# Performance work log

Measured on AMD Instinct MI355X. Metric: run time of the kernel, lower is better.

## Reference

```python
import jax, jax.numpy as jnp
import numpy as np

EPS = 1e-7
TWO_PI = 2.0 * np.pi

K = 4096   # num gaussians
R = 8192   # num rays
MAP_SIZE = 100


def setup_inputs() -> dict:
    key = jax.random.key(0)
    k1, k2, k3, k4, k5, k6 = jax.random.split(key, 6)
    pos_raw = jax.random.normal(k1, (K, 2), dtype=jnp.float32)            # pre-sigmoid positions
    conc_raw = jax.random.normal(k2, (K,), dtype=jnp.float32)             # pre-softplus concentration
    scale_raw = 0.1 * jax.random.normal(k3, (K, 2), dtype=jnp.float32)    # log-scales
    rot_raw = jax.random.uniform(k4, (K,), dtype=jnp.float32) * TWO_PI    # rotation angles
    p_rays = jax.random.uniform(k5, (R, 2), dtype=jnp.float32) * MAP_SIZE # ray origins in map coords
    u = jax.random.normal(k6, (R, 2), dtype=jnp.float32)
    u_rays = u / jnp.linalg.norm(u, axis=-1, keepdims=True)               # unit ray directions
    return {"pos_raw": pos_raw, "conc_raw": conc_raw, "scale_raw": scale_raw,
            "rot_raw": rot_raw, "p_rays": p_rays, "u_rays": u_rays,
            "map_size": MAP_SIZE}


def _forward(pos_raw, conc_raw, scale_raw, rot_raw, p_rays, u_rays, map_size):
    # --- per-gaussian activations (GasSplattingModel getters) ---
    pos = jax.nn.sigmoid(pos_raw) * map_size           # (K,2)
    conc = jax.nn.softplus(conc_raw)                   # (K,)
    scale = jnp.exp(scale_raw)                         # (K,2)
    d0 = 1.0 / (scale[:, 0] ** 2 + EPS)                # diag of S^2 inverse
    d1 = 1.0 / (scale[:, 1] ** 2 + EPS)
    c, s = jnp.cos(rot_raw), jnp.sin(rot_raw)
    # Sigma^{-1} = R diag(d0,d1) R^T with R = [[c,-s],[s,c]]  (symmetric 2x2)
    m00 = c * c * d0 + s * s * d1                      # (K,)
    m01 = c * s * (d0 - d1)
    m11 = s * s * d0 + c * c * d1
    M = jnp.stack([m00, m01, m11], axis=0)             # (3,K) quadratic-form coeffs

    u0, u1 = u_rays[:, 0], u_rays[:, 1]
    p0, p1 = p_rays[:, 0], p_rays[:, 1]

    # quadratic-form features per ray, contracted with M via GEMM -> (R,K)
    qu = jnp.stack([u0 * u0, 2.0 * u0 * u1, u1 * u1], axis=1)        # (R,3)
    qp = jnp.stack([p0 * p0, 2.0 * p0 * p1, p1 * p1], axis=1)        # (R,3)
    qup = jnp.stack([u0 * p0, u0 * p1 + u1 * p0, u1 * p1], axis=1)   # (R,3)
    a = qu @ M          # u^T S u      (R,K)
    pSp = qp @ M        # p^T S p      (R,K)
    uSp = qup @ M       # u^T S p      (R,K)

    # S @ mu per gaussian -> (2,K)
    Sm = jnp.stack([m00 * pos[:, 0] + m01 * pos[:, 1],
                    m01 * pos[:, 0] + m11 * pos[:, 1]], axis=0)
    uSm = u_rays @ Sm   # u^T S mu     (R,K)
    pSm = p_rays @ Sm   # p^T S mu     (R,K)
    mSm = pos[:, 0] * Sm[0] + pos[:, 1] * Sm[1]        # mu^T S mu (K,)

    b = uSp - uSm                                      # u^T S (p - mu)
    c0 = pSp - 2.0 * pSm + mSm[None, :]                # (p-mu)^T S (p-mu)

    # closed-form line integral of conc * exp(-0.5 (x-mu)^T S (x-mu)) along ray
    dens = conc[None, :] * jnp.sqrt(TWO_PI / a) * jnp.exp(-0.5 * (c0 - b * b / a))
    return jnp.sum(dens, axis=-1)                      # (R,)


def reference(pos_raw, conc_raw, scale_raw, rot_raw, p_rays, u_rays, map_size):
    return _forward(pos_raw, conc_raw, scale_raw, rot_raw, p_rays, u_rays, map_size)
```

## Files before the change

kernel.cpp:

```cpp
#include <hip/hip_runtime.h>
#include <hip/hip_bf16.h>

#define EPS 1e-07f

#define BLOCK  256
#define NCH    64
#define PBLOCK 64

#define SQRT_HALF_LOG2E 0.84932180028801904f
#define LOG2_SQRT_2PI   1.32574806473616588f

typedef float v4f __attribute__((ext_vector_type(4)));

__global__ __launch_bounds__(PBLOCK) void precompute_gauss(
                                 const float* __restrict__ pos_raw,
                                 const float* __restrict__ conc_raw,
                                 const float* __restrict__ scale_raw,
                                 const float* __restrict__ rot_raw,
                                 const void*  __restrict__ map_size_p,
                                 float* __restrict__ gG,
                                 float* __restrict__ out,
                                 int K, int KPAD, int R)
{
    int k = blockIdx.x * blockDim.x + threadIdx.x;
    int nthreads = gridDim.x * blockDim.x;

    for (int i = k; i < R; i += nthreads) out[i] = 0.0f;

    if (k >= KPAD) return;

    const int q = k >> 2, e = k & 3;
    float* rec = gG + q * 24;

    if (k >= K) {
        rec[0  + e] = 1.0f;
        rec[4  + e] = 0.0f;
        rec[8  + e] = 1.0f;
        rec[12 + e] = -1e38f;
        rec[16 + e] = 0.0f;
        rec[20 + e] = 0.0f;
        return;
    }

    unsigned int msbits = *(const unsigned int*)map_size_p;
    float msf = __uint_as_float(msbits);
    const float ms = (msf >= 1e-3f && msf <= 1e9f) ? msf
                                                   : (float)(*(const int*)map_size_p);

    float pr0 = pos_raw[2*k],  pr1 = pos_raw[2*k+1];
    float pos0 = ms / (1.0f + __expf(-pr0));
    float pos1 = ms / (1.0f + __expf(-pr1));

    float cr = conc_raw[k];
    float conc = fmaxf(cr, 0.0f) + __logf(1.0f + __expf(-fabsf(cr)));

    float s0 = __expf(scale_raw[2*k]);
    float s1 = __expf(scale_raw[2*k+1]);
    float d0 = 1.0f / (s0*s0 + EPS);
    float d1 = 1.0f / (s1*s1 + EPS);

    float rot = rot_raw[k];
    float c = __cosf(rot), s = __sinf(rot);

    float m00 = c*c*d0 + s*s*d1;
    float m01 = c*s*(d0 - d1);
    float m11 = s*s*d0 + c*c*d1;

    float det    = d0 * d1;
    float invdet = 1.0f / det;
    float cc = __log2f(conc) + LOG2_SQRT_2PI - 0.5f * __log2f(det);

    rec[0  + e] = m00 * invdet;
    rec[4  + e] = m01 * invdet;
    rec[8  + e] = m11 * invdet;
    rec[12 + e] = cc;
    rec[16 + e] = pos0;
    rec[20 + e] = pos1;
}

__global__ __launch_bounds__(BLOCK) void splat_main(
        const float* __restrict__ p_rays,
        const float* __restrict__ u_rays,
        const float* __restrict__ gG,
        float* __restrict__ out,
        int GPC, int R)
{
    const int ray = blockIdx.x * BLOCK + threadIdx.x;

    float2 p2 = *(const float2*)(p_rays + 2*min(ray, R-1));
    float2 u2 = *(const float2*)(u_rays + 2*min(ray, R-1));
    const float p0 = p2.x, p1 = p2.y, u0 = u2.x, u1 = u2.y;

    const float qu0  = u0*u0, qu1 = 2.0f*u0*u1, qu2 = u1*u1;
    const float wt   =  SQRT_HALF_LOG2E * (u0*p1 - u1*p0);
    const float su1  =  SQRT_HALF_LOG2E * u1;
    const float nsu0 = -SQRT_HALF_LOG2E * u0;

    float acc = 0.0f;

    const float* gptr = gG + (size_t)blockIdx.y * GPC * 24;

    for (int g = 0; g < GPC; ++g) {
        v4f M00, M01, M11, CC, P0, P1;
        asm volatile(
            "s_load_dwordx4 %0, %6, 0x0\n\t"
            "s_load_dwordx4 %1, %6, 0x10\n\t"
            "s_load_dwordx4 %2, %6, 0x20\n\t"
            "s_load_dwordx4 %3, %6, 0x30\n\t"
            "s_load_dwordx4 %4, %6, 0x40\n\t"
            "s_load_dwordx4 %5, %6, 0x50\n\t"
            "s_waitcnt lgkmcnt(0)"
            : "=&s"(M00), "=&s"(M01), "=&s"(M11),
              "=&s"(CC),  "=&s"(P0),  "=&s"(P1)
            : "s"(gptr));

        #pragma unroll
        for (int e = 0; e < 4; ++e) {
            float a_  = fmaf(qu2, M11[e], fmaf(qu1, M01[e], qu0 * M00[e]));
            float cr_ = fmaf(nsu0, P1[e], fmaf(su1, P0[e], wt));
            float ra_ = __builtin_amdgcn_rsqf(a_);
            float t_  = cr_ * ra_;
            float ar_ = fmaf(-t_, t_, CC[e]);
            float e_  = __builtin_amdgcn_exp2f(ar_);
            acc = fmaf(ra_, e_, acc);
        }
        gptr += 24;
    }

    if (ray < R) atomicAdd(&out[ray], acc);
}

extern "C" void kernel_launch(void* const* d_in, const int* in_sizes, int n_in,
                              void* d_out, int out_size, void* d_ws, size_t ws_size,
                              hipStream_t stream)
{
    const float* pos_raw   = (const float*)d_in[0];
    const float* conc_raw  = (const float*)d_in[1];
    const float* scale_raw = (const float*)d_in[2];
    const float* rot_raw   = (const float*)d_in[3];
    const float* p_rays    = (const float*)d_in[4];
    const float* u_rays    = (const float*)d_in[5];
    const void*  map_size  = d_in[6];

    const int K = in_sizes[1];
    const int R = out_size;

    const int ng_tot = (K + 3) / 4;
    const int GPC    = (ng_tot + NCH - 1) / NCH;
    const int ng_pad = GPC * NCH;
    const int KPAD   = ng_pad * 4;

    float* out = (float*)d_out;
    float* gG  = (float*)d_ws;

    {
        dim3 grid((KPAD + PBLOCK - 1) / PBLOCK);
        precompute_gauss<<<grid, PBLOCK, 0, stream>>>(pos_raw, conc_raw, scale_raw,
                                                      rot_raw, map_size,
                                                      gG, out, K, KPAD, R);
    }
    {
        dim3 grid((R + BLOCK - 1) / BLOCK, NCH);
        splat_main<<<grid, BLOCK, 0, stream>>>(p_rays, u_rays, gG, out, GPC, R);
    }
}
```

Measured before the change: 23.56 us.

## Stage gaussian slices in LDS and split each ray across 16 gaussian chunks

The main kernel now loads a 1024-gaussian slice into shared memory and has each 512-thread block handle 32 rays. Every half-wave covers a different sub-chunk of the slice, and partial sums are reduced through a shuffle plus a shared-memory pass before one atomic per ray. This replaces the per-iteration scalar loads, each followed by a waitcnt stall, with LDS broadcast reads and cuts the number of global atomics. The cost is a block-wide sync, a larger LDS footprint, and redundant per-ray setup work, since each ray's data is loaded by 16 threads.

```diff
diff --git a/kernel.cpp b/kernel.cpp
--- a/kernel.cpp
+++ b/kernel.cpp
@@ -3,9 +3,12 @@
 
 #define EPS 1e-07f
 
-#define BLOCK  256
-#define NCH    64
-#define PBLOCK 64
+#define BLOCK   512
+#define RPB     32
+#define SLICE_G 1024
+#define NGRP    (SLICE_G/4)
+#define NW      (BLOCK/64)
+#define PBLOCK  64
 
 #define SQRT_HALF_LOG2E 0.84932180028801904f
 #define LOG2_SQRT_2PI   1.32574806473616588f
@@ -83,36 +86,50 @@
         const float* __restrict__ u_rays,
         const float* __restrict__ gG,
         float* __restrict__ out,
-        int GPC, int R)
+        int R)
 {
-    const int ray = blockIdx.x * BLOCK + threadIdx.x;
+    __shared__ v4f  sG4[NGRP * 6];
+    __shared__ float psum[NW][RPB];
 
-    float2 p2 = *(const float2*)(p_rays + 2*min(ray, R-1));
-    float2 u2 = *(const float2*)(u_rays + 2*min(ray, R-1));
+    const int tid   = threadIdx.x;
+    const int lane  = tid & 63;
+    const int wv    = tid >> 6;
+    const int rayl  = lane & 31;
+    const int half  = lane >> 5;
+    const int chunk = (wv << 1) | half;
+    const int NG    = NGRP / 16;
+
+    int ray = blockIdx.x * RPB + rayl;
+    if (ray >= R) ray = R - 1;
+
+    {
+        const v4f* src = (const v4f*)(gG + (size_t)blockIdx.y * NGRP * 24);
+        #pragma unroll
+        for (int i = 0; i < (NGRP * 6) / BLOCK; ++i)
+            sG4[tid + i * BLOCK] = src[tid + i * BLOCK];
+    }
+
+    float2 p2 = *(const float2*)(p_rays + 2*ray);
+    float2 u2 = *(const float2*)(u_rays + 2*ray);
     const float p0 = p2.x, p1 = p2.y, u0 = u2.x, u1 = u2.y;
-
     const float qu0  = u0*u0, qu1 = 2.0f*u0*u1, qu2 = u1*u1;
     const float wt   =  SQRT_HALF_LOG2E * (u0*p1 - u1*p0);
     const float su1  =  SQRT_HALF_LOG2E * u1;
     const float nsu0 = -SQRT_HALF_LOG2E * u0;
 
+    __syncthreads();
+
     float acc = 0.0f;
-
-    const float* gptr = gG + (size_t)blockIdx.y * GPC * 24;
-
-    for (int g = 0; g < GPC; ++g) {
-        v4f M00, M01, M11, CC, P0, P1;
-        asm volatile(
-            "s_load_dwordx4 %0, %6, 0x0\n\t"
-            "s_load_dwordx4 %1, %6, 0x10\n\t"
-            "s_load_dwordx4 %2, %6, 0x20\n\t"
-            "s_load_dwordx4 %3, %6, 0x30\n\t"
-            "s_load_dwordx4 %4, %6, 0x40\n\t"
-            "s_load_dwordx4 %5, %6, 0x50\n\t"
-            "s_waitcnt lgkmcnt(0)"
-            : "=&s"(M00), "=&s"(M01), "=&s"(M11),
-              "=&s"(CC),  "=&s"(P0),  "=&s"(P1)
-            : "s"(gptr));
+    const int g0 = chunk * NG;
+    #pragma unroll 4
+    for (int gq = 0; gq < NG; ++gq) {
+        const v4f* g = &sG4[(g0 + gq) * 6];
+        v4f M00 = g[0];
+        v4f M01 = g[1];
+        v4f M11 = g[2];
+        v4f CC  = g[3];
+        v4f P0  = g[4];
+        v4f P1  = g[5];
 
         #pragma unroll
         for (int e = 0; e < 4; ++e) {
@@ -124,10 +141,19 @@
             float e_  = __builtin_amdgcn_exp2f(ar_);
             acc = fmaf(ra_, e_, acc);
         }
-        gptr += 24;
     }
 
-    if (ray < R) atomicAdd(&out[ray], acc);
+    acc += __shfl_xor(acc, 32, 64);
+    if (half == 0) psum[wv][rayl] = acc;
+    __syncthreads();
+
+    if (wv == 0 && lane < RPB) {
+        float s = 0.0f;
+        #pragma unroll
+        for (int w = 0; w < NW; ++w) s += psum[w][lane];
+        int oray = blockIdx.x * RPB + lane;
+        if (oray < R) atomicAdd(&out[oray], s);
+    }
 }
 
 extern "C" void kernel_launch(void* const* d_in, const int* in_sizes, int n_in,
@@ -145,10 +171,8 @@
     const int K = in_sizes[1];
     const int R = out_size;
 
-    const int ng_tot = (K + 3) / 4;
-    const int GPC    = (ng_tot + NCH - 1) / NCH;
-    const int ng_pad = GPC * NCH;
-    const int KPAD   = ng_pad * 4;
+    const int NSLICE = (K + SLICE_G - 1) / SLICE_G;
+    const int KPAD   = NSLICE * SLICE_G;
 
     float* out = (float*)d_out;
     float* gG  = (float*)d_ws;
@@ -160,7 +184,7 @@
                                                       gG, out, K, KPAD, R);
     }
     {
-        dim3 grid((R + BLOCK - 1) / BLOCK, NCH);
-        splat_main<<<grid, BLOCK, 0, stream>>>(p_rays, u_rays, gG, out, GPC, R);
+        dim3 grid((R + RPB - 1) / RPB, NSLICE);
+        splat_main<<<grid, BLOCK, 0, stream>>>(p_rays, u_rays, gG, out, R);
     }
 }
```

New measurement: 21.65 us. 1.09x faster.
